# Kernel tuning notes

Measured on AMD Instinct MI355X. Metric: run time of the kernel, lower is better.

## Reference

```python
import jax, jax.numpy as jnp
import numpy as np

MARGIN = 1.0
B, D_FEAT = 4096, 256


def setup_inputs() -> dict:
    key = jax.random.key(0)
    return {"inputs": jax.random.normal(key, (B, D_FEAT), dtype=jnp.float32)}


def reference(inputs):
    bsz = inputs.shape[0]
    P = bsz // 2  # number of positive pairs
    # pairwise similarity, scaled as in the original (/128.0)
    D = jnp.matmul(inputs, inputs.T) / 128.0          # [B, B]
    Dexpm = jnp.exp(MARGIN + D)                        # [B, B]

    # Row 2p over odd columns (2k+1), row 2p+1 over even columns (2l)
    Rodd = Dexpm[0::2, 1::2]                           # [P, P]: Dexpm[2p, 2k+1]
    Reven = Dexpm[1::2, 0::2]                          # [P, P]: Dexpm[2p+1, 2l]

    p = jnp.arange(P)
    k = jnp.arange(P)
    # Faithful to the original code's exclusion bug: k != pos_j (=2p+1), l != pos_i (=2p)
    mask_i = (k[None, :] != (2 * p + 1)[:, None]).astype(Dexpm.dtype)  # [P, P]
    mask_j = (k[None, :] != (2 * p)[:, None]).astype(Dexpm.dtype)      # [P, P]

    neg_ik = jnp.sum(Rodd * mask_i, axis=1)            # [P]
    neg_jl = jnp.sum(Reven * mask_j, axis=1)           # [P]

    Dpos = D[2 * p, 2 * p + 1]                         # [P] positive-pair similarity
    J = jnp.log(1e-8 + neg_ik + neg_jl) - Dpos         # [P]
    return jnp.sum(jnp.maximum(J, 0.0) ** 2) / bsz
```

## Files before the change

kernel.cpp:

```cpp
#include <hip/hip_runtime.h>

#define PN 2048

typedef __attribute__((ext_vector_type(8))) short short8;
typedef __attribute__((ext_vector_type(4))) float f32x4;

static __device__ __forceinline__ unsigned int pk_bf2(float lo, float hi) {
    unsigned int ul = __float_as_uint(lo);
    unsigned int uh = __float_as_uint(hi);
    ul = (ul + 0x7fffu + ((ul >> 16) & 1u)) >> 16;
    uh = (uh + 0x7fffu + ((uh >> 16) & 1u)) >> 16;
    return ul | (uh << 16);
}


__global__ __launch_bounds__(512, 2) void sml_mfma(
    const float* __restrict__ X, float* __restrict__ Srow, float* __restrict__ Scol,
    float* __restrict__ Dpos, float* __restrict__ Ex1, float* __restrict__ Ex2)
{
    __shared__ __align__(16) unsigned int A_s[128 * 32];
    __shared__ __align__(16) unsigned int B_s[128 * 32];
    __shared__ float red[4][128];

    const int bx = blockIdx.x, by = blockIdx.y;
    const int t = threadIdx.x;
    const int lane = t & 63, wid = t >> 6;
    const int wr = wid >> 2, wc = wid & 3;
    const int g4 = lane >> 4, rl = lane & 15;

    const int s  = t & 7;
    const int r0 = t >> 3;

    const float* aptr[2];
    const float* bptr[2];
    #pragma unroll
    for (int q = 0; q < 2; ++q) {
        const int r = r0 + 64 * q;
        aptr[q] = X + (size_t)(2 * (bx * 128 + r)) * 256 + s * 8;
        bptr[q] = X + (size_t)(2 * (by * 128 + r) + 1) * 256 + s * 8;
    }

    f32x4 acc[4][2];
    #pragma unroll
    for (int i = 0; i < 4; ++i)
        #pragma unroll
        for (int j = 0; j < 2; ++j) acc[i][j] = (f32x4){0.f, 0.f, 0.f, 0.f};

    float4 pa[2][2], pb[2][2];
    #pragma unroll
    for (int q = 0; q < 2; ++q) {
        pa[q][0] = *(const float4*)(aptr[q]);
        pa[q][1] = *(const float4*)(aptr[q] + 4);
        pb[q][0] = *(const float4*)(bptr[q]);
        pb[q][1] = *(const float4*)(bptr[q] + 4);
    }

    for (int ks = 0; ks < 4; ++ks) {
        __syncthreads();
        #pragma unroll
        for (int q = 0; q < 2; ++q) {
            const int r  = r0 + 64 * q;
            const int sw = (s ^ (r & 7)) << 2;
            uint4 wa = { pk_bf2(pa[q][0].x, pa[q][0].y), pk_bf2(pa[q][0].z, pa[q][0].w),
                         pk_bf2(pa[q][1].x, pa[q][1].y), pk_bf2(pa[q][1].z, pa[q][1].w) };
            uint4 wb = { pk_bf2(pb[q][0].x, pb[q][0].y), pk_bf2(pb[q][0].z, pb[q][0].w),
                         pk_bf2(pb[q][1].x, pb[q][1].y), pk_bf2(pb[q][1].z, pb[q][1].w) };
            *(uint4*)&A_s[r * 32 + sw] = wa;
            *(uint4*)&B_s[r * 32 + sw] = wb;
        }
        __syncthreads();
        if (ks < 3) {
            const int off = (ks + 1) * 64;
            #pragma unroll
            for (int q = 0; q < 2; ++q) {
                pa[q][0] = *(const float4*)(aptr[q] + off);
                pa[q][1] = *(const float4*)(aptr[q] + off + 4);
                pb[q][0] = *(const float4*)(bptr[q] + off);
                pb[q][1] = *(const float4*)(bptr[q] + off + 4);
            }
        }
        #pragma unroll
        for (int kk = 0; kk < 2; ++kk) {
            short8 af[4], bfj[2];
            #pragma unroll
            for (int i = 0; i < 4; ++i) {
                const int r  = wr * 64 + i * 16 + rl;
                const int sl = (kk * 4 + g4) ^ (r & 7);
                af[i] = *(const short8*)&A_s[r * 32 + sl * 4];
            }
            #pragma unroll
            for (int j = 0; j < 2; ++j) {
                const int r  = wc * 32 + j * 16 + rl;
                const int sl = (kk * 4 + g4) ^ (r & 7);
                bfj[j] = *(const short8*)&B_s[r * 32 + sl * 4];
            }
            #pragma unroll
            for (int i = 0; i < 4; ++i)
                #pragma unroll
                for (int j = 0; j < 2; ++j)
                    acc[i][j] = __builtin_amdgcn_mfma_f32_16x16x32_bf16(af[i], bfj[j], acc[i][j], 0, 0, 0);
        }
    }

    float rs[4][4];
    float cs[2] = {0.f, 0.f};
    #pragma unroll
    for (int i = 0; i < 4; ++i)
        #pragma unroll
        for (int rg = 0; rg < 4; ++rg) rs[i][rg] = 0.f;

    #pragma unroll
    for (int i = 0; i < 4; ++i) {
        #pragma unroll
        for (int j = 0; j < 2; ++j) {
            const int kg = by * 128 + wc * 32 + j * 16 + rl;
            #pragma unroll
            for (int rg = 0; rg < 4; ++rg) {
                const int pg = bx * 128 + wr * 64 + i * 16 + g4 * 4 + rg;
                const float c = acc[i][j][rg] * (1.f / 128.f);
                const float e = __expf(1.f + c);
                if (kg == pg) Dpos[pg] = c;
                if (kg == 2 * pg + 1) Ex1[pg] = e;
                if (pg == 2 * kg) Ex2[kg] = e;
                rs[i][rg] += e;
                cs[j] += e;
            }
        }
    }

    #pragma unroll
    for (int i = 0; i < 4; ++i) {
        #pragma unroll
        for (int rg = 0; rg < 4; ++rg) {
            float v = rs[i][rg];
            v += __shfl_xor(v, 1); v += __shfl_xor(v, 2);
            v += __shfl_xor(v, 4); v += __shfl_xor(v, 8);
            if (rl == 0) red[wc][wr * 64 + i * 16 + g4 * 4 + rg] = v;
        }
    }
    __syncthreads();
    if (t < 128)
        Srow[by * PN + bx * 128 + t] = red[0][t] + red[1][t] + red[2][t] + red[3][t];
    __syncthreads();

    #pragma unroll
    for (int j = 0; j < 2; ++j) {
        float v = cs[j];
        v += __shfl_xor(v, 16); v += __shfl_xor(v, 32);
        if (g4 == 0) red[wr][wc * 32 + j * 16 + rl] = v;
    }
    __syncthreads();
    if (t < 128)
        Scol[bx * PN + by * 128 + t] = red[0][t] + red[1][t];
}

__global__ __launch_bounds__(1024) void sml_finish(
    const float* __restrict__ Srow, const float* __restrict__ Scol,
    const float* __restrict__ Dpos, const float* __restrict__ Ex1,
    const float* __restrict__ Ex2, float* __restrict__ out)
{
    __shared__ float red[16];
    const int t = threadIdx.x;
    float local = 0.f;
    for (int p = t; p < PN; p += 1024) {
        float ssum = 0.f;
        #pragma unroll
        for (int g = 0; g < 16; ++g) ssum += Srow[g * PN + p];
        #pragma unroll
        for (int g = 0; g < 16; ++g) ssum += Scol[g * PN + p];
        if (p < 1024) ssum -= Ex1[p] + Ex2[p];
        const float J = __logf(1e-8f + ssum) - Dpos[p];
        const float v = fmaxf(J, 0.f);
        local += v * v;
    }
    #pragma unroll
    for (int m = 1; m < 64; m <<= 1) local += __shfl_xor(local, m);
    if ((t & 63) == 0) red[t >> 6] = local;
    __syncthreads();
    if (t == 0) {
        float ssum = 0.f;
        #pragma unroll
        for (int w = 0; w < 16; ++w) ssum += red[w];
        out[0] = ssum * (1.f / 4096.f);
    }
}

extern "C" void kernel_launch(void* const* d_in, const int* in_sizes, int n_in,
                              void* d_out, int out_size, void* d_ws, size_t ws_size,
                              hipStream_t stream) {
    const float* X = (const float*)d_in[0];
    float* ws   = (float*)d_ws;
    float* Srow = ws;
    float* Scol = Srow + 16 * PN;
    float* Dpos = Scol + 16 * PN;
    float* Ex1  = Dpos + PN;
    float* Ex2  = Ex1 + PN;
    float* out  = (float*)d_out;

    dim3 g1(16, 16);
    sml_mfma<<<g1, dim3(512), 0, stream>>>(X, Srow, Scol, Dpos, Ex1, Ex2);
    sml_finish<<<1, dim3(1024), 0, stream>>>(Srow, Scol, Dpos, Ex1, Ex2, out);
}
```

Baseline: 19.84 us.

## Halve MFMA tile columns to double grid, parallelize finish with atomics

```diff
diff --git a/kernel.cpp b/kernel.cpp
--- a/kernel.cpp
+++ b/kernel.cpp
@@ -14,31 +14,35 @@
 }
 
 
-__global__ __launch_bounds__(512, 2) void sml_mfma(
+__global__ __launch_bounds__(256, 2) void sml_mfma(
     const float* __restrict__ X, float* __restrict__ Srow, float* __restrict__ Scol,
-    float* __restrict__ Dpos, float* __restrict__ Ex1, float* __restrict__ Ex2)
+    float* __restrict__ Dpos, float* __restrict__ Ex1, float* __restrict__ Ex2,
+    float* __restrict__ out)
 {
     __shared__ __align__(16) unsigned int A_s[128 * 32];
-    __shared__ __align__(16) unsigned int B_s[128 * 32];
-    __shared__ float red[4][128];
+    __shared__ __align__(16) unsigned int B_s[64 * 32];
+    __shared__ float red[2][128];
+    __shared__ float red2[2][64];
 
     const int bx = blockIdx.x, by = blockIdx.y;
     const int t = threadIdx.x;
     const int lane = t & 63, wid = t >> 6;
-    const int wr = wid >> 2, wc = wid & 3;
+    const int wr = wid >> 1, wc = wid & 1;
     const int g4 = lane >> 4, rl = lane & 15;
+
+    if (bx == 0 && by == 0 && t == 0) out[0] = 0.f;
 
     const int s  = t & 7;
     const int r0 = t >> 3;
 
-    const float* aptr[2];
+    const float* aptr[4];
     const float* bptr[2];
     #pragma unroll
-    for (int q = 0; q < 2; ++q) {
-        const int r = r0 + 64 * q;
-        aptr[q] = X + (size_t)(2 * (bx * 128 + r)) * 256 + s * 8;
-        bptr[q] = X + (size_t)(2 * (by * 128 + r) + 1) * 256 + s * 8;
-    }
+    for (int q = 0; q < 4; ++q)
+        aptr[q] = X + (size_t)(2 * (bx * 128 + r0 + 32 * q)) * 256 + s * 8;
+    #pragma unroll
+    for (int q = 0; q < 2; ++q)
+        bptr[q] = X + (size_t)(2 * (by * 64 + r0 + 32 * q) + 1) * 256 + s * 8;
 
     f32x4 acc[4][2];
     #pragma unroll
@@ -46,11 +50,14 @@
         #pragma unroll
         for (int j = 0; j < 2; ++j) acc[i][j] = (f32x4){0.f, 0.f, 0.f, 0.f};
 
-    float4 pa[2][2], pb[2][2];
-    #pragma unroll
-    for (int q = 0; q < 2; ++q) {
+    float4 pa[4][2], pb[2][2];
+    #pragma unroll
+    for (int q = 0; q < 4; ++q) {
         pa[q][0] = *(const float4*)(aptr[q]);
         pa[q][1] = *(const float4*)(aptr[q] + 4);
+    }
+    #pragma unroll
+    for (int q = 0; q < 2; ++q) {
         pb[q][0] = *(const float4*)(bptr[q]);
         pb[q][1] = *(const float4*)(bptr[q] + 4);
     }
@@ -58,23 +65,31 @@
     for (int ks = 0; ks < 4; ++ks) {
         __syncthreads();
         #pragma unroll
-        for (int q = 0; q < 2; ++q) {
-            const int r  = r0 + 64 * q;
+        for (int q = 0; q < 4; ++q) {
+            const int r  = r0 + 32 * q;
             const int sw = (s ^ (r & 7)) << 2;
             uint4 wa = { pk_bf2(pa[q][0].x, pa[q][0].y), pk_bf2(pa[q][0].z, pa[q][0].w),
                          pk_bf2(pa[q][1].x, pa[q][1].y), pk_bf2(pa[q][1].z, pa[q][1].w) };
+            *(uint4*)&A_s[r * 32 + sw] = wa;
+        }
+        #pragma unroll
+        for (int q = 0; q < 2; ++q) {
+            const int r  = r0 + 32 * q;
+            const int sw = (s ^ (r & 7)) << 2;
             uint4 wb = { pk_bf2(pb[q][0].x, pb[q][0].y), pk_bf2(pb[q][0].z, pb[q][0].w),
                          pk_bf2(pb[q][1].x, pb[q][1].y), pk_bf2(pb[q][1].z, pb[q][1].w) };
-            *(uint4*)&A_s[r * 32 + sw] = wa;
             *(uint4*)&B_s[r * 32 + sw] = wb;
         }
         __syncthreads();
         if (ks < 3) {
             const int off = (ks + 1) * 64;
             #pragma unroll
-            for (int q = 0; q < 2; ++q) {
+            for (int q = 0; q < 4; ++q) {
                 pa[q][0] = *(const float4*)(aptr[q] + off);
                 pa[q][1] = *(const float4*)(aptr[q] + off + 4);
+            }
+            #pragma unroll
+            for (int q = 0; q < 2; ++q) {
                 pb[q][0] = *(const float4*)(bptr[q] + off);
                 pb[q][1] = *(const float4*)(bptr[q] + off + 4);
             }
@@ -113,7 +128,7 @@
     for (int i = 0; i < 4; ++i) {
         #pragma unroll
         for (int j = 0; j < 2; ++j) {
-            const int kg = by * 128 + wc * 32 + j * 16 + rl;
+            const int kg = by * 64 + wc * 32 + j * 16 + rl;
             #pragma unroll
             for (int rg = 0; rg < 4; ++rg) {
                 const int pg = bx * 128 + wr * 64 + i * 16 + g4 * 4 + rg;
@@ -138,51 +153,38 @@
             if (rl == 0) red[wc][wr * 64 + i * 16 + g4 * 4 + rg] = v;
         }
     }
-    __syncthreads();
-    if (t < 128)
-        Srow[by * PN + bx * 128 + t] = red[0][t] + red[1][t] + red[2][t] + red[3][t];
-    __syncthreads();
-
     #pragma unroll
     for (int j = 0; j < 2; ++j) {
         float v = cs[j];
         v += __shfl_xor(v, 16); v += __shfl_xor(v, 32);
-        if (g4 == 0) red[wr][wc * 32 + j * 16 + rl] = v;
+        if (g4 == 0) red2[wr][wc * 32 + j * 16 + rl] = v;
     }
     __syncthreads();
     if (t < 128)
-        Scol[bx * PN + by * 128 + t] = red[0][t] + red[1][t];
-}
-
-__global__ __launch_bounds__(1024) void sml_finish(
+        Srow[by * PN + bx * 128 + t] = red[0][t] + red[1][t];
+    else if (t < 192)
+        Scol[bx * PN + by * 64 + (t - 128)] = red2[0][t - 128] + red2[1][t - 128];
+}
+
+__global__ __launch_bounds__(64) void sml_finish(
     const float* __restrict__ Srow, const float* __restrict__ Scol,
     const float* __restrict__ Dpos, const float* __restrict__ Ex1,
     const float* __restrict__ Ex2, float* __restrict__ out)
 {
-    __shared__ float red[16];
     const int t = threadIdx.x;
-    float local = 0.f;
-    for (int p = t; p < PN; p += 1024) {
-        float ssum = 0.f;
-        #pragma unroll
-        for (int g = 0; g < 16; ++g) ssum += Srow[g * PN + p];
-        #pragma unroll
-        for (int g = 0; g < 16; ++g) ssum += Scol[g * PN + p];
-        if (p < 1024) ssum -= Ex1[p] + Ex2[p];
-        const float J = __logf(1e-8f + ssum) - Dpos[p];
-        const float v = fmaxf(J, 0.f);
-        local += v * v;
-    }
+    const int p = blockIdx.x * 64 + t;
+    float ssum = 0.f;
+    #pragma unroll
+    for (int g = 0; g < 32; ++g) ssum += Srow[g * PN + p];
+    #pragma unroll
+    for (int g = 0; g < 16; ++g) ssum += Scol[g * PN + p];
+    if (p < 1024) ssum -= Ex1[p] + Ex2[p];
+    const float J = __logf(1e-8f + ssum) - Dpos[p];
+    const float v = fmaxf(J, 0.f);
+    float local = v * v;
     #pragma unroll
     for (int m = 1; m < 64; m <<= 1) local += __shfl_xor(local, m);
-    if ((t & 63) == 0) red[t >> 6] = local;
-    __syncthreads();
-    if (t == 0) {
-        float ssum = 0.f;
-        #pragma unroll
-        for (int w = 0; w < 16; ++w) ssum += red[w];
-        out[0] = ssum * (1.f / 4096.f);
-    }
+    if (t == 0) atomicAdd(out, local * (1.f / 4096.f));
 }
 
 extern "C" void kernel_launch(void* const* d_in, const int* in_sizes, int n_in,
@@ -191,13 +193,13 @@
     const float* X = (const float*)d_in[0];
     float* ws   = (float*)d_ws;
     float* Srow = ws;
-    float* Scol = Srow + 16 * PN;
+    float* Scol = Srow + 32 * PN;
     float* Dpos = Scol + 16 * PN;
     float* Ex1  = Dpos + PN;
     float* Ex2  = Ex1 + PN;
     float* out  = (float*)d_out;
 
-    dim3 g1(16, 16);
-    sml_mfma<<<g1, dim3(512), 0, stream>>>(X, Srow, Scol, Dpos, Ex1, Ex2);
-    sml_finish<<<1, dim3(1024), 0, stream>>>(Srow, Scol, Dpos, Ex1, Ex2, out);
-}
+    dim3 g1(16, 32);
+    sml_mfma<<<g1, dim3(256), 0, stream>>>(X, Srow, Scol, Dpos, Ex1, Ex2, out);
+    sml_finish<<<32, dim3(64), 0, stream>>>(Srow, Scol, Dpos, Ex1, Ex2, out);
+}
```

New measurement: 19.60 us. No clear change (-1.2%).

## Fuse final reduction into GEMM kernel via last-block atomic counter

Applied to the files above, without the earlier changes.

```diff
diff --git a/kernel.cpp b/kernel.cpp
--- a/kernel.cpp
+++ b/kernel.cpp
@@ -14,13 +14,14 @@
 }
 
 
-__global__ __launch_bounds__(512, 2) void sml_mfma(
+__global__ __launch_bounds__(512, 2) void sml_fused(
     const float* __restrict__ X, float* __restrict__ Srow, float* __restrict__ Scol,
-    float* __restrict__ Dpos, float* __restrict__ Ex1, float* __restrict__ Ex2)
+    float* __restrict__ Dpos, unsigned int* __restrict__ cnt, float* __restrict__ out)
 {
     __shared__ __align__(16) unsigned int A_s[128 * 32];
     __shared__ __align__(16) unsigned int B_s[128 * 32];
     __shared__ float red[4][128];
+    __shared__ unsigned int lastflag;
 
     const int bx = blockIdx.x, by = blockIdx.y;
     const int t = threadIdx.x;
@@ -119,11 +120,10 @@
                 const int pg = bx * 128 + wr * 64 + i * 16 + g4 * 4 + rg;
                 const float c = acc[i][j][rg] * (1.f / 128.f);
                 const float e = __expf(1.f + c);
-                if (kg == pg) Dpos[pg] = c;
-                if (kg == 2 * pg + 1) Ex1[pg] = e;
-                if (pg == 2 * kg) Ex2[kg] = e;
-                rs[i][rg] += e;
-                cs[j] += e;
+                if (kg == pg)
+                    __hip_atomic_store(&Dpos[pg], c, __ATOMIC_RELAXED, __HIP_MEMORY_SCOPE_AGENT);
+                rs[i][rg] += (kg == 2 * pg + 1) ? 0.f : e;
+                cs[j]     += (pg == 2 * kg)     ? 0.f : e;
             }
         }
     }
@@ -140,7 +140,9 @@
     }
     __syncthreads();
     if (t < 128)
-        Srow[by * PN + bx * 128 + t] = red[0][t] + red[1][t] + red[2][t] + red[3][t];
+        __hip_atomic_store(&Srow[by * PN + bx * 128 + t],
+                           red[0][t] + red[1][t] + red[2][t] + red[3][t],
+                           __ATOMIC_RELAXED, __HIP_MEMORY_SCOPE_AGENT);
     __syncthreads();
 
     #pragma unroll
@@ -151,37 +153,43 @@
     }
     __syncthreads();
     if (t < 128)
-        Scol[bx * PN + by * 128 + t] = red[0][t] + red[1][t];
-}
-
-__global__ __launch_bounds__(1024) void sml_finish(
-    const float* __restrict__ Srow, const float* __restrict__ Scol,
-    const float* __restrict__ Dpos, const float* __restrict__ Ex1,
-    const float* __restrict__ Ex2, float* __restrict__ out)
-{
-    __shared__ float red[16];
-    const int t = threadIdx.x;
-    float local = 0.f;
-    for (int p = t; p < PN; p += 1024) {
-        float ssum = 0.f;
-        #pragma unroll
-        for (int g = 0; g < 16; ++g) ssum += Srow[g * PN + p];
-        #pragma unroll
-        for (int g = 0; g < 16; ++g) ssum += Scol[g * PN + p];
-        if (p < 1024) ssum -= Ex1[p] + Ex2[p];
-        const float J = __logf(1e-8f + ssum) - Dpos[p];
-        const float v = fmaxf(J, 0.f);
-        local += v * v;
-    }
-    #pragma unroll
-    for (int m = 1; m < 64; m <<= 1) local += __shfl_xor(local, m);
-    if ((t & 63) == 0) red[t >> 6] = local;
+        __hip_atomic_store(&Scol[bx * PN + by * 128 + t],
+                           red[0][t] + red[1][t],
+                           __ATOMIC_RELAXED, __HIP_MEMORY_SCOPE_AGENT);
+
     __syncthreads();
     if (t == 0) {
-        float ssum = 0.f;
-        #pragma unroll
-        for (int w = 0; w < 16; ++w) ssum += red[w];
-        out[0] = ssum * (1.f / 4096.f);
+        unsigned int old = __hip_atomic_fetch_add(cnt, 1u, __ATOMIC_RELAXED, __HIP_MEMORY_SCOPE_AGENT);
+        lastflag = (old == 255u) ? 1u : 0u;
+    }
+    __syncthreads();
+    if (lastflag) {
+        float local = 0.f;
+        #pragma unroll
+        for (int i = 0; i < 4; ++i) {
+            const int p = t + 512 * i;
+            float neg = 0.f;
+            #pragma unroll
+            for (int g = 0; g < 16; ++g)
+                neg += __hip_atomic_load(&Srow[g * PN + p], __ATOMIC_RELAXED, __HIP_MEMORY_SCOPE_AGENT);
+            #pragma unroll
+            for (int g = 0; g < 16; ++g)
+                neg += __hip_atomic_load(&Scol[g * PN + p], __ATOMIC_RELAXED, __HIP_MEMORY_SCOPE_AGENT);
+            const float dp = __hip_atomic_load(&Dpos[p], __ATOMIC_RELAXED, __HIP_MEMORY_SCOPE_AGENT);
+            const float J = __logf(1e-8f + neg) - dp;
+            const float v = fmaxf(J, 0.f);
+            local += v * v;
+        }
+        #pragma unroll
+        for (int m = 1; m < 64; m <<= 1) local += __shfl_xor(local, m);
+        if (lane == 0) red[0][wid] = local;
+        __syncthreads();
+        if (t == 0) {
+            float ssum = 0.f;
+            #pragma unroll
+            for (int w = 0; w < 8; ++w) ssum += red[0][w];
+            out[0] = ssum * (1.f / 4096.f);
+        }
     }
 }
 
@@ -190,14 +198,13 @@
                               hipStream_t stream) {
     const float* X = (const float*)d_in[0];
     float* ws   = (float*)d_ws;
-    float* Srow = ws;
+    unsigned int* cnt = (unsigned int*)ws;
+    float* Srow = ws + 64;
     float* Scol = Srow + 16 * PN;
     float* Dpos = Scol + 16 * PN;
-    float* Ex1  = Dpos + PN;
-    float* Ex2  = Ex1 + PN;
     float* out  = (float*)d_out;
 
+    hipMemsetAsync(cnt, 0, sizeof(unsigned int), stream);
     dim3 g1(16, 16);
-    sml_mfma<<<g1, dim3(512), 0, stream>>>(X, Srow, Scol, Dpos, Ex1, Ex2);
-    sml_finish<<<1, dim3(1024), 0, stream>>>(Srow, Scol, Dpos, Ex1, Ex2, out);
+    sml_fused<<<g1, dim3(512), 0, stream>>>(X, Srow, Scol, Dpos, cnt, out);
 }
```

Result: slower. 25.52 us (+28.7%).

## Fuse finish reduction into cooperative kernel with grid sync and atomic output

Applied to the files above, without the earlier changes.

```diff
diff --git a/kernel.cpp b/kernel.cpp
--- a/kernel.cpp
+++ b/kernel.cpp
@@ -1,4 +1,7 @@
 #include <hip/hip_runtime.h>
+#include <hip/hip_cooperative_groups.h>
+
+namespace cg = cooperative_groups;
 
 #define PN 2048
 
@@ -14,9 +17,9 @@
 }
 
 
-__global__ __launch_bounds__(512, 2) void sml_mfma(
+__global__ __launch_bounds__(512, 1) void sml_coop(
     const float* __restrict__ X, float* __restrict__ Srow, float* __restrict__ Scol,
-    float* __restrict__ Dpos, float* __restrict__ Ex1, float* __restrict__ Ex2)
+    float* __restrict__ Dpos, float* __restrict__ out)
 {
     __shared__ __align__(16) unsigned int A_s[128 * 32];
     __shared__ __align__(16) unsigned int B_s[128 * 32];
@@ -27,6 +30,8 @@
     const int lane = t & 63, wid = t >> 6;
     const int wr = wid >> 2, wc = wid & 3;
     const int g4 = lane >> 4, rl = lane & 15;
+
+    if (bx == 0 && by == 0 && t == 0) out[0] = 0.f;
 
     const int s  = t & 7;
     const int r0 = t >> 3;
@@ -120,10 +125,8 @@
                 const float c = acc[i][j][rg] * (1.f / 128.f);
                 const float e = __expf(1.f + c);
                 if (kg == pg) Dpos[pg] = c;
-                if (kg == 2 * pg + 1) Ex1[pg] = e;
-                if (pg == 2 * kg) Ex2[kg] = e;
-                rs[i][rg] += e;
-                cs[j] += e;
+                rs[i][rg] += (kg == 2 * pg + 1) ? 0.f : e;
+                cs[j]     += (pg == 2 * kg)     ? 0.f : e;
             }
         }
     }
@@ -152,36 +155,28 @@
     __syncthreads();
     if (t < 128)
         Scol[bx * PN + by * 128 + t] = red[0][t] + red[1][t];
-}
 
-__global__ __launch_bounds__(1024) void sml_finish(
-    const float* __restrict__ Srow, const float* __restrict__ Scol,
-    const float* __restrict__ Dpos, const float* __restrict__ Ex1,
-    const float* __restrict__ Ex2, float* __restrict__ out)
-{
-    __shared__ float red[16];
-    const int t = threadIdx.x;
-    float local = 0.f;
-    for (int p = t; p < PN; p += 1024) {
-        float ssum = 0.f;
-        #pragma unroll
-        for (int g = 0; g < 16; ++g) ssum += Srow[g * PN + p];
-        #pragma unroll
-        for (int g = 0; g < 16; ++g) ssum += Scol[g * PN + p];
-        if (p < 1024) ssum -= Ex1[p] + Ex2[p];
-        const float J = __logf(1e-8f + ssum) - Dpos[p];
-        const float v = fmaxf(J, 0.f);
-        local += v * v;
+    cg::this_grid().sync();
+
+    const int b = by * 16 + bx;
+    const int p = b * 8 + wid;
+    float v32 = 0.f;
+    if (lane < 16)       v32 = Srow[lane * PN + p];
+    else if (lane < 32)  v32 = Scol[(lane - 16) * PN + p];
+    v32 += __shfl_xor(v32, 1); v32 += __shfl_xor(v32, 2);
+    v32 += __shfl_xor(v32, 4); v32 += __shfl_xor(v32, 8);
+    v32 += __shfl_xor(v32, 16);
+    if (lane == 0) {
+        const float J = __logf(1e-8f + v32) - Dpos[p];
+        const float m = fmaxf(J, 0.f);
+        red[0][wid] = m * m;
     }
-    #pragma unroll
-    for (int m = 1; m < 64; m <<= 1) local += __shfl_xor(local, m);
-    if ((t & 63) == 0) red[t >> 6] = local;
     __syncthreads();
     if (t == 0) {
         float ssum = 0.f;
         #pragma unroll
-        for (int w = 0; w < 16; ++w) ssum += red[w];
-        out[0] = ssum * (1.f / 4096.f);
+        for (int w = 0; w < 8; ++w) ssum += red[0][w];
+        atomicAdd(out, ssum * (1.f / 4096.f));
     }
 }
 
@@ -193,11 +188,9 @@
     float* Srow = ws;
     float* Scol = Srow + 16 * PN;
     float* Dpos = Scol + 16 * PN;
-    float* Ex1  = Dpos + PN;
-    float* Ex2  = Ex1 + PN;
     float* out  = (float*)d_out;
 
-    dim3 g1(16, 16);
-    sml_mfma<<<g1, dim3(512), 0, stream>>>(X, Srow, Scol, Dpos, Ex1, Ex2);
-    sml_finish<<<1, dim3(1024), 0, stream>>>(Srow, Scol, Dpos, Ex1, Ex2, out);
+    void* args[] = { (void*)&X, (void*)&Srow, (void*)&Scol, (void*)&Dpos, (void*)&out };
+    hipLaunchCooperativeKernel(reinterpret_cast<void*>(sml_coop),
+                               dim3(16, 16), dim3(512), args, 0, stream);
 }
```

Measured after the change: 53.27 us. 169% more time.
